# Kernel tuning notes

Hardware: AMD Instinct MI355X
Metric: run time of the kernel (lower is better)

Reference implementation:

```python
import jax, jax.numpy as jnp
import numpy as np

B, L, D, H, NL = 2, 2048, 1024, 8, 2
HD = D // H
EPS = 1e-8


def layernorm(x, g, b):
    m = jnp.mean(x, axis=-1, keepdims=True)
    v = jnp.mean((x - m) ** 2, axis=-1, keepdims=True)
    return (x - m) / jnp.sqrt(v + EPS) * g + b


def rope(x):
    # x: [B, H, L, HD]; interleaved even/odd rotation as in the torch module
    Ls, Dh = x.shape[-2], x.shape[-1]
    pos = jnp.arange(Ls, dtype=jnp.float32)
    freqs = 1.0 / (10000.0 ** (jnp.arange(0, Dh, 2, dtype=jnp.float32) / Dh))
    ang = pos[:, None] * freqs[None, :]  # [L, HD/2]
    sin, cos = jnp.sin(ang), jnp.cos(ang)
    x1, x2 = x[..., ::2], x[..., 1::2]
    r1 = x1 * cos - x2 * sin
    r2 = x1 * sin + x2 * cos
    return jnp.stack([r1, r2], axis=-1).reshape(x.shape)


def setup_inputs() -> dict:
    key = jax.random.key(0)
    ks = jax.random.split(key, 16)
    s = 0.02

    def w(k, shape):
        return jax.random.normal(k, shape, dtype=jnp.float32) * s

    inp = {
        'seqs': jax.random.normal(ks[0], (B, L, D), dtype=jnp.float32),
        'attn_mask': jnp.broadcast_to(jnp.tril(jnp.ones((L, L), dtype=bool)), (B, L, L)),
        'Wq': w(ks[1], (NL, D, D)), 'bq': jnp.zeros((NL, D), jnp.float32),
        'Wk': w(ks[2], (NL, D, D)), 'bk': jnp.zeros((NL, D), jnp.float32),
        'Wu': w(ks[3], (NL, D, D)), 'bu': jnp.zeros((NL, D), jnp.float32),
        'Wv': w(ks[4], (NL, D, D)), 'bv': jnp.zeros((NL, D), jnp.float32),
        'Wo': w(ks[5], (NL, D, D)), 'bo': jnp.zeros((NL, D), jnp.float32),
        'W1': w(ks[6], (NL, D, D)), 'b1': jnp.zeros((NL, D), jnp.float32),
        'W2': w(ks[7], (NL, D, D)), 'b2': jnp.zeros((NL, D), jnp.float32),
        'ln1_g': jnp.ones((NL, D), jnp.float32), 'ln1_b': jnp.zeros((NL, D), jnp.float32),
        'ln2_g': jnp.ones((NL, D), jnp.float32), 'ln2_b': jnp.zeros((NL, D), jnp.float32),
        'lnf_g': jnp.ones((D,), jnp.float32), 'lnf_b': jnp.zeros((D,), jnp.float32),
    }
    return inp


def reference(seqs, attn_mask, Wq, bq, Wk, bk, Wu, bu, Wv, bv, Wo, bo,
              W1, b1, W2, b2, ln1_g, ln1_b, ln2_g, ln2_b, lnf_g, lnf_b):
    x = seqs
    Bsz, Ls, Dm = x.shape
    mask4 = attn_mask[:, None, :, :]  # [B,1,L,L]
    for i in range(NL):
        h = layernorm(x, ln1_g[i], ln1_b[i])

        def proj(Wm, bm):
            t = jnp.einsum('bld,od->blo', h, Wm) + bm
            return t.reshape(Bsz, Ls, H, HD).transpose(0, 2, 1, 3)

        Q = rope(proj(Wq[i], bq[i]))
        K = rope(proj(Wk[i], bk[i]))
        U = proj(Wu[i], bu[i])
        V = proj(Wv[i], bv[i])
        scores = jnp.einsum('bhqd,bhkd->bhqk', Q, K) / jnp.sqrt(jnp.float32(HD))
        scores = jnp.where(mask4, scores, jnp.float32(-1e9))
        wts = jax.nn.silu(scores)  # SiLU replaces softmax (HSTU)
        a = jnp.einsum('bhqk,bhkd->bhqd', wts, V) * U  # U-gated output
        a = a.transpose(0, 2, 1, 3).reshape(Bsz, Ls, Dm)
        a = jnp.einsum('bld,od->blo', a, Wo[i]) + bo[i]
        x = x + a
        h2 = layernorm(x, ln2_g[i], ln2_b[i])
        p = jnp.einsum('bld,od->blo', h2, W1[i]) + b1[i]
        f = jnp.einsum('bld,od->blo', p * jax.nn.silu(p), W2[i]) + b2[i]  # SwiGLU-style
        x = x + f
    return layernorm(x, lnf_g, lnf_b)
```

## Files before the change

### kernel.cpp

```cpp
#include <hip/hip_runtime.h>
#include <stdint.h>

typedef __attribute__((ext_vector_type(4))) float f32x4;
typedef __attribute__((ext_vector_type(8))) short s16x8;

#define D_ 1024
#define LQ 2048
#define HH_ 8
#define HD_ 128

static __device__ __forceinline__ float bf2f(ushort u){
  union { unsigned int i; float f; } v; v.i = ((unsigned int)u) << 16; return v.f;
}
static __device__ __forceinline__ ushort f2bf(float f){
  union { float f; unsigned int i; } v; v.f = f;
  unsigned int r = v.i + 0x7fffu + ((v.i >> 16) & 1u);
  return (ushort)(r >> 16);
}

struct WP { const float* s[7]; };
__global__ __launch_bounds__(256) void convert_weights(WP wp, ushort* __restrict__ dst){
  int w = blockIdx.x >> 7, blk = blockIdx.x & 127, t = threadIdx.x;
  const float4* s = (const float4*)wp.s[w];
  ushort4* d = (ushort4*)(dst + (size_t)w * 1048576);
  int base = blk * 2048 + t;
  #pragma unroll
  for (int r = 0; r < 8; r++){
    float4 v = s[base + r * 256];
    ushort4 o; o.x = f2bf(v.x); o.y = f2bf(v.y); o.z = f2bf(v.z); o.w = f2bf(v.w);
    d[base + r * 256] = o;
  }
}

template<int OUTF>
__global__ __launch_bounds__(256) void ln_kernel(const float* __restrict__ x,
    const float* __restrict__ g, const float* __restrict__ bb,
    float* __restrict__ outf, ushort* __restrict__ outb){
  int row = blockIdx.x, t = threadIdx.x;
  const float4* xr = (const float4*)(x + (size_t)row * D_);
  float4 v = xr[t];
  float s = v.x + v.y + v.z + v.w;
  float sq = v.x*v.x + v.y*v.y + v.z*v.z + v.w*v.w;
  #pragma unroll
  for (int o = 32; o; o >>= 1){ s += __shfl_down(s, o, 64); sq += __shfl_down(sq, o, 64); }
  __shared__ float red[8];
  int lane = t & 63, wv = t >> 6;
  if (!lane){ red[wv] = s; red[wv + 4] = sq; }
  __syncthreads();
  float S = red[0] + red[1] + red[2] + red[3];
  float SQ = red[4] + red[5] + red[6] + red[7];
  float m = S * (1.f / 1024.f);
  float var = SQ * (1.f / 1024.f) - m * m;
  float inv = rsqrtf(var + 1e-8f);
  float4 gv = ((const float4*)g)[t], bv = ((const float4*)bb)[t];
  float4 y;
  y.x = (v.x - m) * inv * gv.x + bv.x;
  y.y = (v.y - m) * inv * gv.y + bv.y;
  y.z = (v.z - m) * inv * gv.z + bv.z;
  y.w = (v.w - m) * inv * gv.w + bv.w;
  if (OUTF){
    ((float4*)outf)[(size_t)row * 256 + t] = y;
  } else {
    ushort4 o4; o4.x = f2bf(y.x); o4.y = f2bf(y.y); o4.z = f2bf(y.z); o4.w = f2bf(y.w);
    ((ushort4*)outb)[(size_t)row * 256 + t] = o4;
  }
}

struct P4 { ushort* d[4]; const float* b[4]; };

template<int EPI, int NB>
__global__ __launch_bounds__(256, 2) void gemm_k(
    const ushort* __restrict__ A, const ushort* __restrict__ W,
    P4 io, const float* __restrict__ resid, float* __restrict__ outf){
  __shared__ ushort As[128 * 64];
  __shared__ ushort Bs[128 * 64];
  int m0 = (blockIdx.x / NB) << 7;
  int n0 = (blockIdx.x % NB) << 7;
  int t = threadIdx.x, lane = t & 63, wv = t >> 6;
  int l15 = lane & 15, quad = lane >> 4;
  int wm = (wv & 1) << 6, wn = (wv >> 1) << 6;
  f32x4 acc[4][4] = {};
  for (int k0 = 0; k0 < 1024; k0 += 64){
    #pragma unroll
    for (int r = 0; r < 4; r++){
      int cb = r * 256 + wv * 64;
      int c = cb + lane;
      int row = c >> 3, j = c & 7;
      int kk = ((j ^ (row & 7)) << 3);
      __builtin_amdgcn_global_load_lds(
          (const __attribute__((address_space(1))) unsigned int*)(A + (size_t)(m0 + row) * 1024 + k0 + kk),
          (__attribute__((address_space(3))) unsigned int*)&As[cb * 8], 16, 0, 0);
      __builtin_amdgcn_global_load_lds(
          (const __attribute__((address_space(1))) unsigned int*)(W + (size_t)(n0 + row) * 1024 + k0 + kk),
          (__attribute__((address_space(3))) unsigned int*)&Bs[cb * 8], 16, 0, 0);
    }
    __syncthreads();
    #pragma unroll
    for (int kd = 0; kd < 2; kd++){
      s16x8 afr[4], bfr[4];
      #pragma unroll
      for (int mi = 0; mi < 4; mi++){
        int R = wm + mi * 16 + l15;
        afr[mi] = *(const s16x8*)&As[R * 64 + (((kd << 2) | quad) ^ (R & 7)) * 8];
      }
      #pragma unroll
      for (int ni = 0; ni < 4; ni++){
        int R = wn + ni * 16 + l15;
        bfr[ni] = *(const s16x8*)&Bs[R * 64 + (((kd << 2) | quad) ^ (R & 7)) * 8];
      }
      #pragma unroll
      for (int mi = 0; mi < 4; mi++)
        #pragma unroll
        for (int ni = 0; ni < 4; ni++)
          acc[mi][ni] = __builtin_amdgcn_mfma_f32_16x16x32_bf16(afr[mi], bfr[ni], acc[mi][ni], 0, 0, 0);
    }
    __syncthreads();
  }
  int sel = (EPI == 3) ? (n0 >> 10) : 0;
  ushort* dst = io.d[sel];
  const float* bias = io.b[sel];
  int ncol = (EPI == 3) ? (n0 & 1023) : n0;
  #pragma unroll
  for (int mi = 0; mi < 4; mi++){
    int gm = m0 + wm + mi * 16 + quad * 4;
    #pragma unroll
    for (int ni = 0; ni < 4; ni++){
      int cn = ncol + wn + ni * 16 + l15;
      float bv = bias[cn];
      if (EPI == 3 && sel < 2){
        int i2 = (cn & 127) >> 1;
        float freq = __builtin_amdgcn_exp2f(-0.20762050f * (float)i2);
        int odd = cn & 1;
        #pragma unroll
        for (int r = 0; r < 4; r++){
          float val = acc[mi][ni][r] + bv;
          float pv = __shfl_xor(val, 1, 64);
          int pos = (gm + r) & 2047;
          float ang = (float)pos * freq;
          float sv, cv; __sincosf(ang, &sv, &cv);
          float res = odd ? (pv * sv + val * cv) : (val * cv - pv * sv);
          dst[(size_t)(gm + r) * 1024 + cn] = f2bf(res);
        }
      } else {
        #pragma unroll
        for (int r = 0; r < 4; r++){
          float val = acc[mi][ni][r] + bv;
          size_t o = (size_t)(gm + r) * 1024 + cn;
          if (EPI == 1){ outf[o] = resid[o] + val; }
          else if (EPI == 2){
            float sg = __builtin_amdgcn_rcpf(1.f + __expf(-val));
            dst[o] = f2bf(val * val * sg);
          }
          else { dst[o] = f2bf(val); }
        }
      }
    }
  }
}

template<int EPI>
__global__ __launch_bounds__(256, 2) void gemm_k2(
    const ushort* __restrict__ A, const ushort* __restrict__ W,
    const float* __restrict__ bias, ushort* __restrict__ dst,
    const float* __restrict__ resid, float* __restrict__ outf){
  __shared__ ushort As[64 * 64];
  __shared__ ushort Bs[128 * 64];
  int m0 = (blockIdx.x >> 3) << 6;
  int n0 = (blockIdx.x & 7) << 7;
  int t = threadIdx.x, lane = t & 63, wv = t >> 6;
  int l15 = lane & 15, quad = lane >> 4;
  int wm = (wv & 1) << 5, wn = (wv >> 1) << 6;
  f32x4 acc[2][4] = {};
  for (int k0 = 0; k0 < 1024; k0 += 64){
    #pragma unroll
    for (int r = 0; r < 6; r++){
      int cb = (r < 2 ? r * 256 : (r - 2) * 256) + wv * 64;
      int c = cb + lane;
      int row = c >> 3, j = c & 7;
      int kk = ((j ^ (row & 7)) << 3);
      if (r < 2){
        __builtin_amdgcn_global_load_lds(
            (const __attribute__((address_space(1))) unsigned int*)(A + (size_t)(m0 + row) * 1024 + k0 + kk),
            (__attribute__((address_space(3))) unsigned int*)&As[cb * 8], 16, 0, 0);
      } else {
        __builtin_amdgcn_global_load_lds(
            (const __attribute__((address_space(1))) unsigned int*)(W + (size_t)(n0 + row) * 1024 + k0 + kk),
            (__attribute__((address_space(3))) unsigned int*)&Bs[cb * 8], 16, 0, 0);
      }
    }
    __syncthreads();
    #pragma unroll
    for (int kd = 0; kd < 2; kd++){
      s16x8 afr[2], bfr[4];
      #pragma unroll
      for (int mi = 0; mi < 2; mi++){
        int R = wm + mi * 16 + l15;
        afr[mi] = *(const s16x8*)&As[R * 64 + (((kd << 2) | quad) ^ (R & 7)) * 8];
      }
      #pragma unroll
      for (int ni = 0; ni < 4; ni++){
        int R = wn + ni * 16 + l15;
        bfr[ni] = *(const s16x8*)&Bs[R * 64 + (((kd << 2) | quad) ^ (R & 7)) * 8];
      }
      #pragma unroll
      for (int mi = 0; mi < 2; mi++)
        #pragma unroll
        for (int ni = 0; ni < 4; ni++)
          acc[mi][ni] = __builtin_amdgcn_mfma_f32_16x16x32_bf16(afr[mi], bfr[ni], acc[mi][ni], 0, 0, 0);
    }
    __syncthreads();
  }
  #pragma unroll
  for (int mi = 0; mi < 2; mi++){
    int gm = m0 + wm + mi * 16 + quad * 4;
    #pragma unroll
    for (int ni = 0; ni < 4; ni++){
      int cn = n0 + wn + ni * 16 + l15;
      float bv = bias[cn];
      #pragma unroll
      for (int r = 0; r < 4; r++){
        float val = acc[mi][ni][r] + bv;
        size_t o = (size_t)(gm + r) * 1024 + cn;
        if (EPI == 1){ outf[o] = resid[o] + val; }
        else {
          float sg = __builtin_amdgcn_rcpf(1.f + __expf(-val));
          dst[o] = f2bf(val * val * sg);
        }
      }
    }
  }
}

__global__ __launch_bounds__(256) void transpose_v(const ushort* __restrict__ Vb, ushort* __restrict__ Vt){
  int bidx = blockIdx.x;
  int dt = bidx & 1, lt = (bidx >> 1) & 31, bh = bidx >> 6;
  int b = bh >> 3, hh = bh & 7;
  int l0 = lt << 6, d0 = dt << 6;
  __shared__ ushort tile[64][66];
  int t = threadIdx.x;
  #pragma unroll
  for (int r = 0; r < 8; r++){
    int idx = r * 256 + t;
    int row = idx >> 5, cu = idx & 31;
    unsigned int val = *(const unsigned int*)(Vb + (size_t)(b * LQ + l0 + row) * D_ + hh * HD_ + d0 + cu * 2);
    *(unsigned int*)&tile[row][cu * 2] = val;
  }
  __syncthreads();
  #pragma unroll
  for (int r = 0; r < 8; r++){
    int idx = r * 256 + t;
    int drow = idx >> 5, lu = idx & 31;
    unsigned int val = (unsigned int)tile[lu * 2][drow] | ((unsigned int)tile[lu * 2 + 1][drow] << 16);
    *(unsigned int*)(Vt + ((size_t)(bh * HD_ + d0 + drow)) * LQ + l0 + lu * 2) = val;
  }
}

__global__ __launch_bounds__(256, 3) void attn_kernel(
    const ushort* __restrict__ Q, const ushort* __restrict__ K,
    const ushort* __restrict__ Vt,
    ushort* __restrict__ Po0, ushort* __restrict__ Po1){
  __shared__ ushort Ks[64 * 136];
  __shared__ ushort Vs[128 * 72];
  __shared__ ushort Ps[64 * 72];
  int t = threadIdx.x, lane = t & 63, wv = t >> 6;
  int l15 = lane & 15, quad = lane >> 4, q8 = quad * 8;
  int idx = blockIdx.x;
  int bh = idx & 15;
  int slot = idx >> 4;
  int qt = 31 - (slot >> 1);
  int half = slot & 1;
  int n = qt + 1;
  int c0 = (n + 1) >> 1;
  int klo = half ? c0 : 0;
  int khi = half ? n : c0;
  if (klo >= khi) return;
  int b = bh >> 3, hh = bh & 7;
  int q0 = qt << 6;
  const float scale = 0.08838834764831845f;

  s16x8 qf[4];
  const ushort* qbase = Q + (size_t)(b * LQ + q0 + (wv << 4) + l15) * D_ + hh * HD_;
  #pragma unroll
  for (int kd = 0; kd < 4; kd++) qf[kd] = *(const s16x8*)(qbase + kd * 32 + q8);

  f32x4 acc_o[8] = {};
  for (int kt = klo; kt < khi; kt++){
    int k0 = kt << 6;
    __syncthreads();
    #pragma unroll
    for (int r = 0; r < 4; r++){
      int c = r * 256 + t, row = c >> 4, ck = c & 15;
      *(s16x8*)&Ks[row * 136 + ck * 8] =
          *(const s16x8*)(K + (size_t)(b * LQ + k0 + row) * D_ + hh * HD_ + ck * 8);
    }
    #pragma unroll
    for (int r = 0; r < 4; r++){
      int c = r * 256 + t, row = c >> 3, ck = c & 7;
      *(s16x8*)&Vs[row * 72 + ck * 8] =
          *(const s16x8*)(Vt + (size_t)(bh * HD_ + row) * LQ + k0 + ck * 8);
    }
    __syncthreads();
    f32x4 sacc[4] = {};
    #pragma unroll
    for (int kd = 0; kd < 4; kd++){
      #pragma unroll
      for (int ni = 0; ni < 4; ni++){
        s16x8 bf = *(const s16x8*)&Ks[(ni * 16 + l15) * 136 + kd * 32 + q8];
        sacc[ni] = __builtin_amdgcn_mfma_f32_16x16x32_bf16(qf[kd], bf, sacc[ni], 0, 0, 0);
      }
    }
    int qg0 = q0 + (wv << 4) + quad * 4;
    #pragma unroll
    for (int ni = 0; ni < 4; ni++){
      int kg = k0 + ni * 16 + l15;
      #pragma unroll
      for (int r = 0; r < 4; r++){
        float s = sacc[ni][r] * scale;
        float p = (kg <= qg0 + r) ? (s * __builtin_amdgcn_rcpf(1.f + __expf(-s))) : 0.f;
        Ps[((wv << 4) + quad * 4 + r) * 72 + ni * 16 + l15] = f2bf(p);
      }
    }
    int prow = (wv << 4) + l15;
    #pragma unroll
    for (int kv = 0; kv < 2; kv++){
      s16x8 af = *(const s16x8*)&Ps[prow * 72 + kv * 32 + q8];
      #pragma unroll
      for (int nt = 0; nt < 8; nt++){
        s16x8 bf = *(const s16x8*)&Vs[(nt * 16 + l15) * 72 + kv * 32 + q8];
        acc_o[nt] = __builtin_amdgcn_mfma_f32_16x16x32_bf16(af, bf, acc_o[nt], 0, 0, 0);
      }
    }
  }
  ushort* Po = half ? Po1 : Po0;
  #pragma unroll
  for (int nt = 0; nt < 8; nt++){
    #pragma unroll
    for (int r = 0; r < 4; r++){
      int qg = q0 + (wv << 4) + quad * 4 + r;
      int dd = nt * 16 + l15;
      Po[(size_t)(b * LQ + qg) * D_ + hh * HD_ + dd] = f2bf(acc_o[nt][r]);
    }
  }
}

__global__ __launch_bounds__(256) void attn_reduce(
    const ushort* __restrict__ Po0, const ushort* __restrict__ Po1,
    const ushort* __restrict__ U, ushort* __restrict__ Aout){
  int i = (blockIdx.x * 256 + threadIdx.x) * 4;
  int l = (i >> 10) & 2047;
  ushort4 p0 = *(const ushort4*)(Po0 + i);
  float v0 = bf2f(p0.x), v1 = bf2f(p0.y), v2 = bf2f(p0.z), v3 = bf2f(p0.w);
  if (l >= 64){
    ushort4 p1 = *(const ushort4*)(Po1 + i);
    v0 += bf2f(p1.x); v1 += bf2f(p1.y); v2 += bf2f(p1.z); v3 += bf2f(p1.w);
  }
  ushort4 u = *(const ushort4*)(U + i);
  ushort4 o;
  o.x = f2bf(v0 * bf2f(u.x)); o.y = f2bf(v1 * bf2f(u.y));
  o.z = f2bf(v2 * bf2f(u.z)); o.w = f2bf(v3 * bf2f(u.w));
  *(ushort4*)(Aout + i) = o;
}

extern "C" void kernel_launch(void* const* d_in, const int* in_sizes, int n_in,
                              void* d_out, int out_size, void* d_ws, size_t ws_size,
                              hipStream_t stream){
  const float* seqs = (const float*)d_in[0];
  const float* bq = (const float*)d_in[3];
  const float* bk = (const float*)d_in[5];
  const float* bu = (const float*)d_in[7];
  const float* bv = (const float*)d_in[9];
  const float* bo = (const float*)d_in[11];
  const float* b1 = (const float*)d_in[13];
  const float* b2 = (const float*)d_in[15];
  const float* ln1g = (const float*)d_in[16];
  const float* ln1b = (const float*)d_in[17];
  const float* ln2g = (const float*)d_in[18];
  const float* ln2b = (const float*)d_in[19];
  const float* lnfg = (const float*)d_in[20];
  const float* lnfb = (const float*)d_in[21];

  char* base = (char*)d_ws;
  const size_t MB = 1u << 20;
  if (ws_size < 78 * MB) return;
  ushort* wbf = (ushort*)base;
  ushort* h   = (ushort*)(base + 14 * MB);
  ushort* Qb  = (ushort*)(base + 22 * MB);
  ushort* Kb  = (ushort*)(base + 30 * MB);
  ushort* Ub  = (ushort*)(base + 38 * MB);
  ushort* Vb  = (ushort*)(base + 46 * MB);
  ushort* Vt  = (ushort*)(base + 54 * MB);
  float*  xb  = (float*)(base + 62 * MB);
  ushort* ab  = h;

  const size_t DD = 1048576;
  for (int i = 0; i < 2; i++){
    WP wp;
    for (int j = 0; j < 7; j++)
      wp.s[j] = (const float*)d_in[2 + 2 * j] + (size_t)i * DD;
    convert_weights<<<7 * 128, 256, 0, stream>>>(wp, wbf);
    const ushort* Wl = wbf;
    const float* xin = (i == 0) ? seqs : xb;
    ln_kernel<0><<<4096, 256, 0, stream>>>(xin, ln1g + i * D_, ln1b + i * D_, nullptr, h);
    P4 io_qkuv = {{Qb, Kb, Ub, Vb}, {bq + i * D_, bk + i * D_, bu + i * D_, bv + i * D_}};
    gemm_k<3, 32><<<1024, 256, 0, stream>>>(h, Wl, io_qkuv, nullptr, nullptr);
    transpose_v<<<1024, 256, 0, stream>>>(Vb, Vt);
    attn_kernel<<<1024, 256, 0, stream>>>(Qb, Kb, Vt, ab, Vb);
    attn_reduce<<<4096, 256, 0, stream>>>(ab, Vb, Ub, ab);
    gemm_k2<1><<<512, 256, 0, stream>>>(ab, Wl + 4 * DD, bo + i * D_, nullptr, xin, xb);
    ln_kernel<0><<<4096, 256, 0, stream>>>(xb, ln2g + i * D_, ln2b + i * D_, nullptr, h);
    gemm_k2<2><<<512, 256, 0, stream>>>(h, Wl + 5 * DD, b1 + i * D_, Qb, nullptr, nullptr);
    gemm_k2<1><<<512, 256, 0, stream>>>(Qb, Wl + 6 * DD, b2 + i * D_, nullptr, xb, xb);
  }
  ln_kernel<1><<<4096, 256, 0, stream>>>(xb, lnfg, lnfb, (float*)d_out, nullptr);
}
```

Measured before the change: 505.2 us.

## Use 128-row query tiles in attention with XOR-swizzled LDS and per-wave causal skip

The attention kernel now processes 128 query rows per block (32 per wave, two MFMA row tiles), so each K/V tile loaded into shared memory is reused across twice as many queries, and the grid is halved to 512 blocks. LDS padding is replaced with an XOR swizzle on 8-element chunks to avoid bank conflicts in less shared memory. Waves skip compute on key tiles lying entirely above their causal diagonal. Split halves are now always non-empty, so the reduce kernel drops its branch. The trade-off is higher register pressure from the doubled accumulators and fewer blocks to fill the GPU.

```diff
diff --git a/kernel.cpp b/kernel.cpp
--- a/kernel.cpp
+++ b/kernel.cpp
@@ -259,101 +259,122 @@
     const ushort* __restrict__ Q, const ushort* __restrict__ K,
     const ushort* __restrict__ Vt,
     ushort* __restrict__ Po0, ushort* __restrict__ Po1){
-  __shared__ ushort Ks[64 * 136];
-  __shared__ ushort Vs[128 * 72];
-  __shared__ ushort Ps[64 * 72];
+  __shared__ ushort Ks[64 * 128];
+  __shared__ ushort Vs[128 * 64];
+  __shared__ ushort Ps[128 * 64];
   int t = threadIdx.x, lane = t & 63, wv = t >> 6;
   int l15 = lane & 15, quad = lane >> 4, q8 = quad * 8;
   int idx = blockIdx.x;
   int bh = idx & 15;
   int slot = idx >> 4;
-  int qt = 31 - (slot >> 1);
+  int qt = 15 - (slot >> 1);
   int half = slot & 1;
-  int n = qt + 1;
-  int c0 = (n + 1) >> 1;
+  int nkt = 2 * qt + 2;
+  int c0 = qt + 1;
   int klo = half ? c0 : 0;
-  int khi = half ? n : c0;
-  if (klo >= khi) return;
+  int khi = half ? nkt : c0;
   int b = bh >> 3, hh = bh & 7;
-  int q0 = qt << 6;
+  int q0 = qt << 7;
+  int wq0 = q0 + wv * 32;
   const float scale = 0.08838834764831845f;
 
-  s16x8 qf[4];
-  const ushort* qbase = Q + (size_t)(b * LQ + q0 + (wv << 4) + l15) * D_ + hh * HD_;
-  #pragma unroll
-  for (int kd = 0; kd < 4; kd++) qf[kd] = *(const s16x8*)(qbase + kd * 32 + q8);
-
-  f32x4 acc_o[8] = {};
+  s16x8 qf[2][4];
+  #pragma unroll
+  for (int mi = 0; mi < 2; mi++){
+    const ushort* qbase = Q + (size_t)(b * LQ + wq0 + mi * 16 + l15) * D_ + hh * HD_;
+    #pragma unroll
+    for (int kd = 0; kd < 4; kd++) qf[mi][kd] = *(const s16x8*)(qbase + kd * 32 + q8);
+  }
+
+  f32x4 acc_o[2][8] = {};
   for (int kt = klo; kt < khi; kt++){
     int k0 = kt << 6;
     __syncthreads();
     #pragma unroll
     for (int r = 0; r < 4; r++){
       int c = r * 256 + t, row = c >> 4, ck = c & 15;
-      *(s16x8*)&Ks[row * 136 + ck * 8] =
+      *(s16x8*)&Ks[row * 128 + ((ck ^ (row & 7)) << 3)] =
           *(const s16x8*)(K + (size_t)(b * LQ + k0 + row) * D_ + hh * HD_ + ck * 8);
     }
     #pragma unroll
     for (int r = 0; r < 4; r++){
       int c = r * 256 + t, row = c >> 3, ck = c & 7;
-      *(s16x8*)&Vs[row * 72 + ck * 8] =
+      *(s16x8*)&Vs[row * 64 + ((ck ^ (row & 7)) << 3)] =
           *(const s16x8*)(Vt + (size_t)(bh * HD_ + row) * LQ + k0 + ck * 8);
     }
     __syncthreads();
-    f32x4 sacc[4] = {};
-    #pragma unroll
-    for (int kd = 0; kd < 4; kd++){
-      #pragma unroll
-      for (int ni = 0; ni < 4; ni++){
-        s16x8 bf = *(const s16x8*)&Ks[(ni * 16 + l15) * 136 + kd * 32 + q8];
-        sacc[ni] = __builtin_amdgcn_mfma_f32_16x16x32_bf16(qf[kd], bf, sacc[ni], 0, 0, 0);
-      }
-    }
-    int qg0 = q0 + (wv << 4) + quad * 4;
-    #pragma unroll
-    for (int ni = 0; ni < 4; ni++){
-      int kg = k0 + ni * 16 + l15;
+    if (k0 <= wq0 + 31){
+      f32x4 sacc[2][4] = {};
+      #pragma unroll
+      for (int kd = 0; kd < 4; kd++){
+        s16x8 kfr[4];
+        #pragma unroll
+        for (int ni = 0; ni < 4; ni++){
+          int R = ni * 16 + l15;
+          kfr[ni] = *(const s16x8*)&Ks[R * 128 + ((((kd << 2) | quad) ^ (R & 7)) << 3)];
+        }
+        #pragma unroll
+        for (int mi = 0; mi < 2; mi++)
+          #pragma unroll
+          for (int ni = 0; ni < 4; ni++)
+            sacc[mi][ni] = __builtin_amdgcn_mfma_f32_16x16x32_bf16(qf[mi][kd], kfr[ni], sacc[mi][ni], 0, 0, 0);
+      }
+      #pragma unroll
+      for (int mi = 0; mi < 2; mi++){
+        int qg0 = wq0 + mi * 16 + quad * 4;
+        #pragma unroll
+        for (int ni = 0; ni < 4; ni++){
+          int kg = k0 + ni * 16 + l15;
+          int chunkbase = (ni * 16 + l15) >> 3, coff = l15 & 7;
+          #pragma unroll
+          for (int r = 0; r < 4; r++){
+            float s = sacc[mi][ni][r] * scale;
+            float p = (kg <= qg0 + r) ? (s * __builtin_amdgcn_rcpf(1.f + __expf(-s))) : 0.f;
+            int row = wv * 32 + mi * 16 + quad * 4 + r;
+            Ps[row * 64 + ((chunkbase ^ (row & 7)) << 3) + coff] = f2bf(p);
+          }
+        }
+      }
+      #pragma unroll
+      for (int kv = 0; kv < 2; kv++){
+        s16x8 vfr[8];
+        #pragma unroll
+        for (int nt = 0; nt < 8; nt++){
+          int R = nt * 16 + l15;
+          vfr[nt] = *(const s16x8*)&Vs[R * 64 + ((((kv << 2) | quad) ^ (R & 7)) << 3)];
+        }
+        #pragma unroll
+        for (int mi = 0; mi < 2; mi++){
+          int row = wv * 32 + mi * 16 + l15;
+          s16x8 af = *(const s16x8*)&Ps[row * 64 + ((((kv << 2) | quad) ^ (row & 7)) << 3)];
+          #pragma unroll
+          for (int nt = 0; nt < 8; nt++)
+            acc_o[mi][nt] = __builtin_amdgcn_mfma_f32_16x16x32_bf16(af, vfr[nt], acc_o[mi][nt], 0, 0, 0);
+        }
+      }
+    }
+  }
+  ushort* Po = half ? Po1 : Po0;
+  #pragma unroll
+  for (int mi = 0; mi < 2; mi++)
+    #pragma unroll
+    for (int nt = 0; nt < 8; nt++)
       #pragma unroll
       for (int r = 0; r < 4; r++){
-        float s = sacc[ni][r] * scale;
-        float p = (kg <= qg0 + r) ? (s * __builtin_amdgcn_rcpf(1.f + __expf(-s))) : 0.f;
-        Ps[((wv << 4) + quad * 4 + r) * 72 + ni * 16 + l15] = f2bf(p);
-      }
-    }
-    int prow = (wv << 4) + l15;
-    #pragma unroll
-    for (int kv = 0; kv < 2; kv++){
-      s16x8 af = *(const s16x8*)&Ps[prow * 72 + kv * 32 + q8];
-      #pragma unroll
-      for (int nt = 0; nt < 8; nt++){
-        s16x8 bf = *(const s16x8*)&Vs[(nt * 16 + l15) * 72 + kv * 32 + q8];
-        acc_o[nt] = __builtin_amdgcn_mfma_f32_16x16x32_bf16(af, bf, acc_o[nt], 0, 0, 0);
-      }
-    }
-  }
-  ushort* Po = half ? Po1 : Po0;
-  #pragma unroll
-  for (int nt = 0; nt < 8; nt++){
-    #pragma unroll
-    for (int r = 0; r < 4; r++){
-      int qg = q0 + (wv << 4) + quad * 4 + r;
-      int dd = nt * 16 + l15;
-      Po[(size_t)(b * LQ + qg) * D_ + hh * HD_ + dd] = f2bf(acc_o[nt][r]);
-    }
-  }
+        int qg = wq0 + mi * 16 + quad * 4 + r;
+        int dd = nt * 16 + l15;
+        Po[(size_t)(b * LQ + qg) * D_ + hh * HD_ + dd] = f2bf(acc_o[mi][nt][r]);
+      }
 }
 
 __global__ __launch_bounds__(256) void attn_reduce(
     const ushort* __restrict__ Po0, const ushort* __restrict__ Po1,
     const ushort* __restrict__ U, ushort* __restrict__ Aout){
   int i = (blockIdx.x * 256 + threadIdx.x) * 4;
-  int l = (i >> 10) & 2047;
   ushort4 p0 = *(const ushort4*)(Po0 + i);
-  float v0 = bf2f(p0.x), v1 = bf2f(p0.y), v2 = bf2f(p0.z), v3 = bf2f(p0.w);
-  if (l >= 64){
-    ushort4 p1 = *(const ushort4*)(Po1 + i);
-    v0 += bf2f(p1.x); v1 += bf2f(p1.y); v2 += bf2f(p1.z); v3 += bf2f(p1.w);
-  }
+  ushort4 p1 = *(const ushort4*)(Po1 + i);
+  float v0 = bf2f(p0.x) + bf2f(p1.x), v1 = bf2f(p0.y) + bf2f(p1.y);
+  float v2 = bf2f(p0.z) + bf2f(p1.z), v3 = bf2f(p0.w) + bf2f(p1.w);
   ushort4 u = *(const ushort4*)(U + i);
   ushort4 o;
   o.x = f2bf(v0 * bf2f(u.x)); o.y = f2bf(v1 * bf2f(u.y));
@@ -404,7 +425,7 @@
     P4 io_qkuv = {{Qb, Kb, Ub, Vb}, {bq + i * D_, bk + i * D_, bu + i * D_, bv + i * D_}};
     gemm_k<3, 32><<<1024, 256, 0, stream>>>(h, Wl, io_qkuv, nullptr, nullptr);
     transpose_v<<<1024, 256, 0, stream>>>(Vb, Vt);
-    attn_kernel<<<1024, 256, 0, stream>>>(Qb, Kb, Vt, ab, Vb);
+    attn_kernel<<<512, 256, 0, stream>>>(Qb, Kb, Vt, ab, Vb);
     attn_reduce<<<4096, 256, 0, stream>>>(ab, Vb, Ub, ab);
     gemm_k2<1><<<512, 256, 0, stream>>>(ab, Wl + 4 * DD, bo + i * D_, nullptr, xin, xb);
     ln_kernel<0><<<4096, 256, 0, stream>>>(xb, ln2g + i * D_, ln2b + i * D_, nullptr, h);
```

Measured after the change: 791.1 us. +56.6%, slower.
